# Kernel tuning notes

Hardware: AMD Instinct MI355X
Metric: run time of the kernel (lower is better)

The kernel has to match this reference:

```python
import jax, jax.numpy as jnp
import numpy as np

# Fixed-point emulation: SharedFxpShift = 8 -> scale 256. Integer bit-shifts of the
# original int32/int8 pipeline are emulated in float32 (multiply/divide by 2^8) with
# int8 clamping, keeping the same dataflow (resblock -> pred head -> bin packing ->
# upsample -> (N,8,ch) child scatter) so a quantized kernel can be checked against it.
SHIFT = 256.0

def requant(x):
    # RequantFxpToScaledInt8: shift down and clamp to int8 range
    return jnp.clip(x * (1.0 / SHIFT), -128.0, 127.0)

def prelu(x, a):
    return jnp.where(x >= 0, x, a * x)

def resblock(x, w1, w2, a):
    # SparseResBlockIn32W8Out32: requant -> linear -> prelu -> requant -> linear -> +x
    h = requant(x)
    h = h @ w1.T
    h = prelu(h, a)
    h = requant(h)
    h = h @ w2.T
    return x + h

def setup_inputs() -> dict:
    key = jax.random.key(0)
    ks = jax.random.split(key, 16)
    N, CH = 50000, 256
    w = lambda k, shp: jax.random.normal(k, shp, dtype=jnp.float32) * 0.05
    return {
        'x': jax.random.normal(ks[0], (N, CH), dtype=jnp.float32) * SHIFT,
        'cur_bin': jax.random.randint(ks[1], (N, 8), 0, 2, dtype=jnp.int32),
        'w_dec1': w(ks[2], (CH, CH)),
        'w_dec2': w(ks[3], (CH, CH)),
        'a_dec': jax.random.uniform(ks[4], (1,), dtype=jnp.float32),
        'w_pconv': w(ks[5], (CH, CH)),
        'a_pconv': jax.random.uniform(ks[6], (1,), dtype=jnp.float32),
        'w_plin': w(ks[7], (255, CH)),
        'w_up1': w(ks[8], (CH, CH + 8)),
        'a_up1': jax.random.uniform(ks[9], (1,), dtype=jnp.float32),
        'w_ur1': w(ks[10], (CH, CH)),
        'w_ur2': w(ks[11], (CH, CH)),
        'a_ur': jax.random.uniform(ks[12], (1,), dtype=jnp.float32),
        'w_uout': w(ks[13], (2048, CH)),
    }

def reference(x, cur_bin, w_dec1, w_dec2, a_dec, w_pconv, a_pconv, w_plin,
              w_up1, a_up1, w_ur1, w_ur2, a_ur, w_uout):
    N, CH = x.shape
    binf = cur_bin.astype(jnp.float32)
    # dec: residual block
    rec = resblock(x, w_dec1, w_dec2, a_dec)
    # pred: requant -> conv+prelu -> requant -> linear(ch,255)
    h = requant(rec)
    h = prelu(h @ w_pconv.T, a_pconv)
    h = requant(h)
    cur_pred = h @ w_plin.T                                   # [N, 255]
    # bin -> octree symbol: (cur_bin << arange(8)).sum(1) - 1
    bin2oct = jnp.arange(8, dtype=jnp.int32)
    cur_oct = jnp.sum(cur_bin << bin2oct, axis=1).astype(jnp.int16) - 1  # [N]
    # upsample: cat(rec, bin << shift) -> requant -> lin+prelu -> resblock -> requant -> lin(ch*8)
    u = jnp.concatenate([rec, binf * SHIFT], axis=1)          # [N, CH+8]
    u = requant(u)
    u = prelu(u @ w_up1.T, a_up1)
    u = resblock(u, w_ur1, w_ur2, a_ur)
    u = requant(u)
    u = u @ w_uout.T                                          # [N, 8*CH]
    # child gather: original does reshape(N,8,CH)[cur_bin.bool()] (ragged);
    # we keep the dense [N,8,CH] with unoccupied children zeroed (jit-friendly).
    rec_out = u.reshape(N, 8, CH) * binf[:, :, None]
    return rec_out, cur_pred, cur_oct
```

## Files before the change

kernel.cpp:

```cpp
#include <hip/hip_runtime.h>

typedef __bf16 bf16x8 __attribute__((ext_vector_type(8)));
typedef float  f32x4  __attribute__((ext_vector_type(4)));

#define OFF_DEC1  0
#define OFF_DEC2  65536
#define OFF_PCONV 131072
#define OFF_PLIN  196608
#define OFF_UP1   262144
#define OFF_UR1   335872
#define OFF_UR2   401408
#define OFF_UOUT  466944
#define WB_TOTAL  991232

__device__ __align__(16) unsigned short g_wb[WB_TOTAL];

__device__ __forceinline__ unsigned short f2bf(float f) {
  union { float f; unsigned u; } c; c.f = f;
  unsigned u = c.u + 0x7FFFu + ((c.u >> 16) & 1u);
  return (unsigned short)(u >> 16);
}
__device__ __forceinline__ float bf2f(unsigned short b) {
  union { unsigned u; float f; } c; c.u = ((unsigned)b) << 16;
  return c.f;
}
__device__ __forceinline__ float reqf(float v) {
  return fminf(fmaxf(v * 0.00390625f, -128.f), 127.f);
}

__global__ void wconv_kernel(const float* __restrict__ wd1, const float* __restrict__ wd2,
                             const float* __restrict__ wpc, const float* __restrict__ wpl,
                             const float* __restrict__ wu1, const float* __restrict__ wr1,
                             const float* __restrict__ wr2, const float* __restrict__ wuo) {
  int t = blockIdx.x * 256 + threadIdx.x;
  if (t >= WB_TOTAL) return;
  const float* src; int local, Ksrc = 256, Msrc = 256, rowOff = 0;
  if      (t < OFF_DEC2)  { src = wd1; local = t; }
  else if (t < OFF_PCONV) { src = wd2; local = t - OFF_DEC2; }
  else if (t < OFF_PLIN)  { src = wpc; local = t - OFF_PCONV; }
  else if (t < OFF_UP1)   { src = wpl; local = t - OFF_PLIN; Msrc = 255; }
  else if (t < OFF_UR1)   { src = wu1; local = t - OFF_UP1; Ksrc = 264; }
  else if (t < OFF_UR2)   { src = wr1; local = t - OFF_UR1; }
  else if (t < OFF_UOUT)  { src = wr2; local = t - OFF_UR2; }
  else { local = t - OFF_UOUT; int c = local >> 16; local &= 65535; src = wuo; rowOff = c * 256; }
  const int s = local >> 13, j = local & 8191;
  const int h = j >> 12, wv = (j >> 9) & 7, lq = (j >> 7) & 3;
  const int l15 = (j >> 3) & 15, kk = j & 7;
  const int m = wv * 32 + h * 16 + l15;
  const int k = s * 32 + lq * 8 + kk;
  float v = (m < Msrc && k < Ksrc) ? src[(size_t)(rowOff + m) * Ksrc + k] : 0.f;
  g_wb[t] = f2bf(v);
}


__device__ __forceinline__ void zero_acc(f32x4 (&acc)[2][4]) {
#pragma unroll
  for (int i = 0; i < 2; ++i)
#pragma unroll
    for (int j = 0; j < 4; ++j) acc[i][j] = (f32x4){0.f, 0.f, 0.f, 0.f};
}

__device__ __forceinline__ void prelu_acc(f32x4 (&acc)[2][4], float a) {
#pragma unroll
  for (int i = 0; i < 2; ++i)
#pragma unroll
    for (int j = 0; j < 4; ++j)
#pragma unroll
      for (int r = 0; r < 4; ++r) {
        float v = acc[i][j][r];
        acc[i][j][r] = v >= 0.f ? v : a * v;
      }
}

__device__ __forceinline__ void stageWh(const unsigned short* __restrict__ src,
                                        unsigned short* dst, int w, int l) {
  const int off = w * 512 + l * 8;
  __builtin_amdgcn_global_load_lds(
      (const __attribute__((address_space(1))) unsigned*)(src + off),
      (__attribute__((address_space(3))) unsigned*)(dst + off),
      16, 0, 0);
}

template<int NKS, bool BIN_TAIL>
__device__ __forceinline__ void gemm_ring(const unsigned short* __restrict__ wcur,
                                          const unsigned short* __restrict__ wnext,
                                          unsigned short* sW,
                                          const unsigned short* sAct,
                                          const unsigned short* sBinA,
                                          int w, int l, int l15, int lq,
                                          f32x4 (&acc)[2][4]) {
  bf16x8 af[4];
#pragma unroll
  for (int hs = 0; hs < 2 * NKS; ++hs) {
    const int ks = hs >> 1, mt = hs & 1;
    const int slot = hs & 1, nslot = slot ^ 1;
    if (hs + 1 < 2 * NKS) {
      stageWh(wcur + (hs + 1) * 4096, sW + nslot * 4096, w, l);
      asm volatile("s_waitcnt vmcnt(1)" ::: "memory");
    } else if (wnext) {
      stageWh(wnext, sW + nslot * 4096, w, l);
      asm volatile("s_waitcnt vmcnt(1)" ::: "memory");
    } else {
      asm volatile("s_waitcnt vmcnt(0)" ::: "memory");
    }
    __builtin_amdgcn_sched_barrier(0);
    if (mt == 0) {
      if (BIN_TAIL && ks == NKS - 1) {
#pragma unroll
        for (int nt = 0; nt < 4; ++nt)
          af[nt] = *(const bf16x8*)(sBinA + (nt * 16 + l15) * 32 + lq * 8);
      } else {
        const int kb = ks * 64 + lq * 16;
#pragma unroll
        for (int nt = 0; nt < 4; ++nt) {
          const int row = nt * 16 + l15;
          af[nt] = *(const bf16x8*)((const char*)sAct + row * 512 + (kb ^ ((row & 15) << 4)));
        }
      }
    }
    __builtin_amdgcn_s_setprio(1);
    bf16x8 bfr = *(const bf16x8*)(sW + slot * 4096 + w * 512 + lq * 128 + l15 * 8);
#pragma unroll
    for (int nt = 0; nt < 4; ++nt)
      acc[mt][nt] = __builtin_amdgcn_mfma_f32_16x16x32_bf16(bfr, af[nt], acc[mt][nt], 0, 0, 0);
    __builtin_amdgcn_s_setprio(0);
  }
}

__device__ __forceinline__ void stage_rq(const f32x4 (&acc)[2][4], unsigned short* dst,
                                         int w, int l15, int lq) {
#pragma unroll
  for (int nt = 0; nt < 4; ++nt) {
    const int row = nt * 16 + l15;
    const int swz = (row & 15) << 4;
#pragma unroll
    for (int mt = 0; mt < 2; ++mt) {
      const int ch2 = (w * 32 + mt * 16 + lq * 4) * 2;
      ushort4 b4;
      b4.x = f2bf(reqf(acc[mt][nt][0]));
      b4.y = f2bf(reqf(acc[mt][nt][1]));
      b4.z = f2bf(reqf(acc[mt][nt][2]));
      b4.w = f2bf(reqf(acc[mt][nt][3]));
      *(ushort4*)((char*)dst + row * 512 + (ch2 ^ swz)) = b4;
    }
  }
}

__device__ __forceinline__ void store_chunk(const f32x4 (&acc)[2][4], float* __restrict__ out,
                                            const unsigned short* sBinA, int r0, int N,
                                            int c, int w, int l15, int lq) {
#pragma unroll
  for (int nt = 0; nt < 4; ++nt) {
    const int row = nt * 16 + l15;
    if ((r0 + row) < N) {
      const float m = sBinA[row * 32 + c] ? 1.f : 0.f;
      float* rp = out + (size_t)(r0 + row) * 2048 + c * 256;
#pragma unroll
      for (int mt = 0; mt < 2; ++mt) {
        const int ch0 = w * 32 + mt * 16 + lq * 4;
        f32x4 v;
        v[0] = acc[mt][nt][0] * m; v[1] = acc[mt][nt][1] * m;
        v[2] = acc[mt][nt][2] * m; v[3] = acc[mt][nt][3] * m;
        *(f32x4*)(rp + ch0) = v;
      }
    }
  }
}

__global__ __launch_bounds__(512, 4) void fused_kernel(
    const float* __restrict__ x, const int* __restrict__ cur_bin,
    const float* __restrict__ a_dec, const float* __restrict__ a_pconv,
    const float* __restrict__ a_up1, const float* __restrict__ a_ur,
    float* __restrict__ out, int N)
{
  __shared__ __align__(16) unsigned short sA[64 * 256];
  __shared__ __align__(16) unsigned short sW[2 * 4096];
  __shared__ __align__(16) unsigned short sBinA[64 * 32];

  const int tid = threadIdx.x;
  const int w = tid >> 6, l = tid & 63;
  const int l15 = l & 15, lq = l >> 4;
  const int r0 = blockIdx.x * 64;
  const size_t PRED_BASE = (size_t)N * 2048;
  const size_t OCT_BASE  = PRED_BASE + (size_t)N * 255;

  const float A_DEC = a_dec[0], A_PCONV = a_pconv[0], A_UP1 = a_up1[0], A_UR = a_ur[0];

  stageWh(g_wb + OFF_DEC1, sW, w, l);

  for (int i = tid; i < 64 * 32; i += 512) {
    const int row = i >> 5, j = i & 31;
    float bv = 0.f;
    if (j < 8 && (r0 + row) < N) bv = (float)cur_bin[(size_t)(r0 + row) * 8 + j];
    sBinA[i] = (j < 8) ? f2bf(bv) : (unsigned short)0;
  }
  if (tid < 64 && (r0 + tid) < N) {
    int s = 0;
#pragma unroll
    for (int j = 0; j < 8; ++j) s += cur_bin[(size_t)(r0 + tid) * 8 + j] << j;
    out[OCT_BASE + r0 + tid] = (float)(s - 1);
  }
#pragma unroll
  for (int it = 0; it < 8; ++it) {
    const int e = it * 2048 + tid * 4;
    const int row = e >> 8, col = e & 255;
    float4 xv = make_float4(0.f, 0.f, 0.f, 0.f);
    if ((r0 + row) < N) xv = *(const float4*)(x + (size_t)(r0 + row) * 256 + col);
    ushort4 b4;
    b4.x = f2bf(reqf(xv.x)); b4.y = f2bf(reqf(xv.y));
    b4.z = f2bf(reqf(xv.z)); b4.w = f2bf(reqf(xv.w));
    *(ushort4*)((char*)sA + row * 512 + ((col * 2) ^ ((row & 15) << 4))) = b4;
  }
  __syncthreads();

  f32x4 acc[2][4];

  zero_acc(acc);
  gemm_ring<8, false>(g_wb + OFF_DEC1, g_wb + OFF_DEC2, sW, sA, sBinA, w, l, l15, lq, acc);
  prelu_acc(acc, A_DEC);
  __syncthreads();
  stage_rq(acc, sA, w, l15, lq);
  __syncthreads();

  zero_acc(acc);
  gemm_ring<8, false>(g_wb + OFF_DEC2, g_wb + OFF_UP1, sW, sA, sBinA, w, l, l15, lq, acc);
  __syncthreads();
#pragma unroll
  for (int nt = 0; nt < 4; ++nt) {
    const int row = nt * 16 + l15;
    const int swz = (row & 15) << 4;
#pragma unroll
    for (int mt = 0; mt < 2; ++mt) {
      const int ch0 = w * 32 + mt * 16 + lq * 4;
      float4 xv = make_float4(0.f, 0.f, 0.f, 0.f);
      if ((r0 + row) < N) xv = *(const float4*)(x + (size_t)(r0 + row) * 256 + ch0);
      ushort4 b4;
      b4.x = f2bf(reqf(xv.x + acc[mt][nt][0]));
      b4.y = f2bf(reqf(xv.y + acc[mt][nt][1]));
      b4.z = f2bf(reqf(xv.z + acc[mt][nt][2]));
      b4.w = f2bf(reqf(xv.w + acc[mt][nt][3]));
      *(ushort4*)((char*)sA + row * 512 + ((ch0 * 2) ^ swz)) = b4;
    }
  }
  __syncthreads();

  unsigned u1p[2][4][2];
  zero_acc(acc);
  gemm_ring<9, true>(g_wb + OFF_UP1, g_wb + OFF_PCONV, sW, sA, sBinA, w, l, l15, lq, acc);
  prelu_acc(acc, A_UP1);
#pragma unroll
  for (int i = 0; i < 2; ++i)
#pragma unroll
    for (int j = 0; j < 4; ++j)
#pragma unroll
      for (int p = 0; p < 2; ++p)
        u1p[i][j][p] = (unsigned)f2bf(acc[i][j][2 * p]) |
                       ((unsigned)f2bf(acc[i][j][2 * p + 1]) << 16);

  zero_acc(acc);
  gemm_ring<8, false>(g_wb + OFF_PCONV, g_wb + OFF_PLIN, sW, sA, sBinA, w, l, l15, lq, acc);
  prelu_acc(acc, A_PCONV);
  __syncthreads();
  stage_rq(acc, sA, w, l15, lq);
  __syncthreads();

  zero_acc(acc);
  gemm_ring<8, false>(g_wb + OFF_PLIN, g_wb + OFF_UR1, sW, sA, sBinA, w, l, l15, lq, acc);
#pragma unroll
  for (int nt = 0; nt < 4; ++nt) {
    const int row = nt * 16 + l15;
    if ((r0 + row) < N) {
      float* rp = out + PRED_BASE + (size_t)(r0 + row) * 255;
#pragma unroll
      for (int mt = 0; mt < 2; ++mt) {
        const int col0 = w * 32 + mt * 16 + lq * 4;
#pragma unroll
        for (int r = 0; r < 4; ++r)
          if (col0 + r < 255)
            rp[col0 + r] = acc[mt][nt][r];
      }
    }
  }
  __syncthreads();

#pragma unroll
  for (int nt = 0; nt < 4; ++nt) {
    const int row = nt * 16 + l15;
    const int swz = (row & 15) << 4;
#pragma unroll
    for (int mt = 0; mt < 2; ++mt) {
      const int ch2 = (w * 32 + mt * 16 + lq * 4) * 2;
      ushort4 b4;
      b4.x = f2bf(reqf(bf2f((unsigned short)(u1p[mt][nt][0]))));
      b4.y = f2bf(reqf(bf2f((unsigned short)(u1p[mt][nt][0] >> 16))));
      b4.z = f2bf(reqf(bf2f((unsigned short)(u1p[mt][nt][1]))));
      b4.w = f2bf(reqf(bf2f((unsigned short)(u1p[mt][nt][1] >> 16))));
      *(ushort4*)((char*)sA + row * 512 + (ch2 ^ swz)) = b4;
    }
  }
  __syncthreads();

  zero_acc(acc);
  gemm_ring<8, false>(g_wb + OFF_UR1, g_wb + OFF_UR2, sW, sA, sBinA, w, l, l15, lq, acc);
  prelu_acc(acc, A_UR);
  __syncthreads();
  stage_rq(acc, sA, w, l15, lq);
  __syncthreads();

  zero_acc(acc);
  gemm_ring<8, false>(g_wb + OFF_UR2, g_wb + OFF_UOUT, sW, sA, sBinA, w, l, l15, lq, acc);
#pragma unroll
  for (int i = 0; i < 2; ++i)
#pragma unroll
    for (int j = 0; j < 4; ++j) {
      acc[i][j][0] += bf2f((unsigned short)(u1p[i][j][0]));
      acc[i][j][1] += bf2f((unsigned short)(u1p[i][j][0] >> 16));
      acc[i][j][2] += bf2f((unsigned short)(u1p[i][j][1]));
      acc[i][j][3] += bf2f((unsigned short)(u1p[i][j][1] >> 16));
    }
  __syncthreads();
  stage_rq(acc, sA, w, l15, lq);
  __syncthreads();

#define G8_CHUNK(c, nextptr)                                                            \
  zero_acc(acc);                                                                        \
  gemm_ring<8, false>(g_wb + OFF_UOUT + (c) * 65536, nextptr, sW, sA, sBinA,            \
                      w, l, l15, lq, acc);                                              \
  store_chunk(acc, out, sBinA, r0, N, (c), w, l15, lq);

  G8_CHUNK(0, g_wb + OFF_UOUT + 1 * 65536)
  G8_CHUNK(1, g_wb + OFF_UOUT + 2 * 65536)
  G8_CHUNK(2, g_wb + OFF_UOUT + 3 * 65536)
  G8_CHUNK(3, g_wb + OFF_UOUT + 4 * 65536)
  G8_CHUNK(4, g_wb + OFF_UOUT + 5 * 65536)
  G8_CHUNK(5, g_wb + OFF_UOUT + 6 * 65536)
  G8_CHUNK(6, g_wb + OFF_UOUT + 7 * 65536)
  G8_CHUNK(7, (const unsigned short*)nullptr)
#undef G8_CHUNK
}

extern "C" void kernel_launch(void* const* d_in, const int* in_sizes, int n_in,
                              void* d_out, int out_size, void* d_ws, size_t ws_size,
                              hipStream_t stream) {
  const float* x        = (const float*)d_in[0];
  const int*   cur_bin  = (const int*)d_in[1];
  const float* w_dec1   = (const float*)d_in[2];
  const float* w_dec2   = (const float*)d_in[3];
  const float* a_dec    = (const float*)d_in[4];
  const float* w_pconv  = (const float*)d_in[5];
  const float* a_pconv  = (const float*)d_in[6];
  const float* w_plin   = (const float*)d_in[7];
  const float* w_up1    = (const float*)d_in[8];
  const float* a_up1    = (const float*)d_in[9];
  const float* w_ur1    = (const float*)d_in[10];
  const float* w_ur2    = (const float*)d_in[11];
  const float* a_ur     = (const float*)d_in[12];
  const float* w_uout   = (const float*)d_in[13];

  const int N = in_sizes[0] / 256;

  wconv_kernel<<<(WB_TOTAL + 255) / 256, 256, 0, stream>>>(
      w_dec1, w_dec2, w_pconv, w_plin, w_up1, w_ur1, w_ur2, w_uout);

  fused_kernel<<<(N + 63) / 64, 512, 0, stream>>>(
      x, cur_bin, a_dec, a_pconv, a_up1, a_ur, (float*)d_out, N);
}
```

Measured before the change: 277.4 us.

## Prefetch weights through registers two k-steps ahead instead of async LDS ring

Replaces the per-half-step global_load_lds double buffer with a register-staged pipeline. Each wave loads its weight slice for k-step ks+2 into registers and writes the slice for ks+1 into a private LDS slot. The packed weight layout is reordered so one k-step holds both M sub-tiles per wave, and the weight LDS buffer doubles in size. The aim is to remove the vmcnt waits and sched barriers on every half-step and to overlap global latency with more MFMA work. The cost is extra VGPRs and more LDS per block, which can lower occupancy or cause spills.

```diff
diff --git a/kernel.cpp b/kernel.cpp
--- a/kernel.cpp
+++ b/kernel.cpp
@@ -44,9 +44,9 @@
   else if (t < OFF_UOUT)  { src = wr2; local = t - OFF_UR2; }
   else { local = t - OFF_UOUT; int c = local >> 16; local &= 65535; src = wuo; rowOff = c * 256; }
   const int s = local >> 13, j = local & 8191;
-  const int h = j >> 12, wv = (j >> 9) & 7, lq = (j >> 7) & 3;
+  const int wv = j >> 10, lq = (j >> 8) & 3, mt = (j >> 7) & 1;
   const int l15 = (j >> 3) & 15, kk = j & 7;
-  const int m = wv * 32 + h * 16 + l15;
+  const int m = wv * 32 + mt * 16 + l15;
   const int k = s * 32 + lq * 8 + kk;
   float v = (m < Msrc && k < Ksrc) ? src[(size_t)(rowOff + m) * Ksrc + k] : 0.f;
   g_wb[t] = f2bf(v);
@@ -72,58 +72,51 @@
       }
 }
 
-__device__ __forceinline__ void stageWh(const unsigned short* __restrict__ src,
-                                        unsigned short* dst, int w, int l) {
-  const int off = w * 512 + l * 8;
-  __builtin_amdgcn_global_load_lds(
-      (const __attribute__((address_space(1))) unsigned*)(src + off),
-      (__attribute__((address_space(3))) unsigned*)(dst + off),
-      16, 0, 0);
-}
-
-template<int NKS, bool BIN_TAIL>
-__device__ __forceinline__ void gemm_ring(const unsigned short* __restrict__ wcur,
-                                          const unsigned short* __restrict__ wnext,
-                                          unsigned short* sW,
-                                          const unsigned short* sAct,
-                                          const unsigned short* sBinA,
-                                          int w, int l, int l15, int lq,
-                                          f32x4 (&acc)[2][4]) {
-  bf16x8 af[4];
-#pragma unroll
-  for (int hs = 0; hs < 2 * NKS; ++hs) {
-    const int ks = hs >> 1, mt = hs & 1;
-    const int slot = hs & 1, nslot = slot ^ 1;
-    if (hs + 1 < 2 * NKS) {
-      stageWh(wcur + (hs + 1) * 4096, sW + nslot * 4096, w, l);
-      asm volatile("s_waitcnt vmcnt(1)" ::: "memory");
-    } else if (wnext) {
-      stageWh(wnext, sW + nslot * 4096, w, l);
-      asm volatile("s_waitcnt vmcnt(1)" ::: "memory");
+template<int NKS, bool BIN_TAIL, int PH>
+__device__ __forceinline__ void gemm_rs(const unsigned short* __restrict__ wcur,
+                                        const unsigned short* __restrict__ wnext,
+                                        bf16x8 (&wr)[2][2],
+                                        unsigned short* sW,
+                                        const unsigned short* sAct,
+                                        const unsigned short* sBinA,
+                                        int w, int l, int l15, int lq,
+                                        f32x4 (&acc)[2][4]) {
+  const int off = w * 1024 + l * 8;
+#pragma unroll
+  for (int ks = 0; ks < NKS; ++ks) {
+    const int cur = (PH + ks) & 1;
+    const int nxt = cur ^ 1;
+    if (ks + 1 < NKS || wnext != nullptr) {
+      *(bf16x8*)(sW + nxt * 8192 + off)       = wr[nxt][0];
+      *(bf16x8*)(sW + nxt * 8192 + off + 512) = wr[nxt][1];
+    }
+    const unsigned short* nsrc = nullptr;
+    if (ks + 2 < NKS)      nsrc = wcur + (ks + 2) * 8192;
+    else if (wnext)        nsrc = wnext + (ks + 2 - NKS) * 8192;
+    if (nsrc) {
+      wr[cur][0] = *(const bf16x8*)(nsrc + off);
+      wr[cur][1] = *(const bf16x8*)(nsrc + off + 512);
+    }
+    bf16x8 af[4];
+    if (BIN_TAIL && ks == NKS - 1) {
+#pragma unroll
+      for (int nt = 0; nt < 4; ++nt)
+        af[nt] = *(const bf16x8*)(sBinA + (nt * 16 + l15) * 32 + lq * 8);
     } else {
-      asm volatile("s_waitcnt vmcnt(0)" ::: "memory");
-    }
-    __builtin_amdgcn_sched_barrier(0);
-    if (mt == 0) {
-      if (BIN_TAIL && ks == NKS - 1) {
-#pragma unroll
-        for (int nt = 0; nt < 4; ++nt)
-          af[nt] = *(const bf16x8*)(sBinA + (nt * 16 + l15) * 32 + lq * 8);
-      } else {
-        const int kb = ks * 64 + lq * 16;
-#pragma unroll
-        for (int nt = 0; nt < 4; ++nt) {
-          const int row = nt * 16 + l15;
-          af[nt] = *(const bf16x8*)((const char*)sAct + row * 512 + (kb ^ ((row & 15) << 4)));
-        }
+      const int kb = ks * 64 + lq * 16;
+#pragma unroll
+      for (int nt = 0; nt < 4; ++nt) {
+        const int row = nt * 16 + l15;
+        af[nt] = *(const bf16x8*)((const char*)sAct + row * 512 + (kb ^ ((row & 15) << 4)));
       }
     }
-    __builtin_amdgcn_s_setprio(1);
-    bf16x8 bfr = *(const bf16x8*)(sW + slot * 4096 + w * 512 + lq * 128 + l15 * 8);
-#pragma unroll
-    for (int nt = 0; nt < 4; ++nt)
-      acc[mt][nt] = __builtin_amdgcn_mfma_f32_16x16x32_bf16(bfr, af[nt], acc[mt][nt], 0, 0, 0);
-    __builtin_amdgcn_s_setprio(0);
+#pragma unroll
+    for (int mt = 0; mt < 2; ++mt) {
+      bf16x8 bfr = *(const bf16x8*)(sW + cur * 8192 + w * 1024 + lq * 256 + mt * 128 + l15 * 8);
+#pragma unroll
+      for (int nt = 0; nt < 4; ++nt)
+        acc[mt][nt] = __builtin_amdgcn_mfma_f32_16x16x32_bf16(bfr, af[nt], acc[mt][nt], 0, 0, 0);
+    }
   }
 }
 
@@ -146,27 +139,6 @@
   }
 }
 
-__device__ __forceinline__ void store_chunk(const f32x4 (&acc)[2][4], float* __restrict__ out,
-                                            const unsigned short* sBinA, int r0, int N,
-                                            int c, int w, int l15, int lq) {
-#pragma unroll
-  for (int nt = 0; nt < 4; ++nt) {
-    const int row = nt * 16 + l15;
-    if ((r0 + row) < N) {
-      const float m = sBinA[row * 32 + c] ? 1.f : 0.f;
-      float* rp = out + (size_t)(r0 + row) * 2048 + c * 256;
-#pragma unroll
-      for (int mt = 0; mt < 2; ++mt) {
-        const int ch0 = w * 32 + mt * 16 + lq * 4;
-        f32x4 v;
-        v[0] = acc[mt][nt][0] * m; v[1] = acc[mt][nt][1] * m;
-        v[2] = acc[mt][nt][2] * m; v[3] = acc[mt][nt][3] * m;
-        *(f32x4*)(rp + ch0) = v;
-      }
-    }
-  }
-}
-
 __global__ __launch_bounds__(512, 4) void fused_kernel(
     const float* __restrict__ x, const int* __restrict__ cur_bin,
     const float* __restrict__ a_dec, const float* __restrict__ a_pconv,
@@ -174,7 +146,7 @@
     float* __restrict__ out, int N)
 {
   __shared__ __align__(16) unsigned short sA[64 * 256];
-  __shared__ __align__(16) unsigned short sW[2 * 4096];
+  __shared__ __align__(16) unsigned short sW[2 * 8192];
   __shared__ __align__(16) unsigned short sBinA[64 * 32];
 
   const int tid = threadIdx.x;
@@ -186,7 +158,12 @@
 
   const float A_DEC = a_dec[0], A_PCONV = a_pconv[0], A_UP1 = a_up1[0], A_UR = a_ur[0];
 
-  stageWh(g_wb + OFF_DEC1, sW, w, l);
+  const int woff = w * 1024 + l * 8;
+  bf16x8 wr[2][2];
+  wr[0][0] = *(const bf16x8*)(g_wb + OFF_DEC1 + woff);
+  wr[0][1] = *(const bf16x8*)(g_wb + OFF_DEC1 + woff + 512);
+  wr[1][0] = *(const bf16x8*)(g_wb + OFF_DEC1 + 8192 + woff);
+  wr[1][1] = *(const bf16x8*)(g_wb + OFF_DEC1 + 8192 + woff + 512);
 
   for (int i = tid; i < 64 * 32; i += 512) {
     const int row = i >> 5, j = i & 31;
@@ -200,7 +177,7 @@
     for (int j = 0; j < 8; ++j) s += cur_bin[(size_t)(r0 + tid) * 8 + j] << j;
     out[OCT_BASE + r0 + tid] = (float)(s - 1);
   }
-#pragma unroll
+#pragma unroll 1
   for (int it = 0; it < 8; ++it) {
     const int e = it * 2048 + tid * 4;
     const int row = e >> 8, col = e & 255;
@@ -213,17 +190,20 @@
   }
   __syncthreads();
 
+  *(bf16x8*)(sW + woff)       = wr[0][0];
+  *(bf16x8*)(sW + woff + 512) = wr[0][1];
+
   f32x4 acc[2][4];
 
   zero_acc(acc);
-  gemm_ring<8, false>(g_wb + OFF_DEC1, g_wb + OFF_DEC2, sW, sA, sBinA, w, l, l15, lq, acc);
+  gemm_rs<8, false, 0>(g_wb + OFF_DEC1, g_wb + OFF_DEC2, wr, sW, sA, sBinA, w, l, l15, lq, acc);
   prelu_acc(acc, A_DEC);
   __syncthreads();
   stage_rq(acc, sA, w, l15, lq);
   __syncthreads();
 
   zero_acc(acc);
-  gemm_ring<8, false>(g_wb + OFF_DEC2, g_wb + OFF_UP1, sW, sA, sBinA, w, l, l15, lq, acc);
+  gemm_rs<8, false, 0>(g_wb + OFF_DEC2, g_wb + OFF_UP1, wr, sW, sA, sBinA, w, l, l15, lq, acc);
   __syncthreads();
 #pragma unroll
   for (int nt = 0; nt < 4; ++nt) {
@@ -246,7 +226,7 @@
 
   unsigned u1p[2][4][2];
   zero_acc(acc);
-  gemm_ring<9, true>(g_wb + OFF_UP1, g_wb + OFF_PCONV, sW, sA, sBinA, w, l, l15, lq, acc);
+  gemm_rs<9, true, 0>(g_wb + OFF_UP1, g_wb + OFF_PCONV, wr, sW, sA, sBinA, w, l, l15, lq, acc);
   prelu_acc(acc, A_UP1);
 #pragma unroll
   for (int i = 0; i < 2; ++i)
@@ -258,14 +238,14 @@
                        ((unsigned)f2bf(acc[i][j][2 * p + 1]) << 16);
 
   zero_acc(acc);
-  gemm_ring<8, false>(g_wb + OFF_PCONV, g_wb + OFF_PLIN, sW, sA, sBinA, w, l, l15, lq, acc);
+  gemm_rs<8, false, 1>(g_wb + OFF_PCONV, g_wb + OFF_PLIN, wr, sW, sA, sBinA, w, l, l15, lq, acc);
   prelu_acc(acc, A_PCONV);
   __syncthreads();
   stage_rq(acc, sA, w, l15, lq);
   __syncthreads();
 
   zero_acc(acc);
-  gemm_ring<8, false>(g_wb + OFF_PLIN, g_wb + OFF_UR1, sW, sA, sBinA, w, l, l15, lq, acc);
+  gemm_rs<8, false, 1>(g_wb + OFF_PLIN, g_wb + OFF_UR1, wr, sW, sA, sBinA, w, l, l15, lq, acc);
 #pragma unroll
   for (int nt = 0; nt < 4; ++nt) {
     const int row = nt * 16 + l15;
@@ -301,14 +281,14 @@
   __syncthreads();
 
   zero_acc(acc);
-  gemm_ring<8, false>(g_wb + OFF_UR1, g_wb + OFF_UR2, sW, sA, sBinA, w, l, l15, lq, acc);
+  gemm_rs<8, false, 1>(g_wb + OFF_UR1, g_wb + OFF_UR2, wr, sW, sA, sBinA, w, l, l15, lq, acc);
   prelu_acc(acc, A_UR);
   __syncthreads();
   stage_rq(acc, sA, w, l15, lq);
   __syncthreads();
 
   zero_acc(acc);
-  gemm_ring<8, false>(g_wb + OFF_UR2, g_wb + OFF_UOUT, sW, sA, sBinA, w, l, l15, lq, acc);
+  gemm_rs<8, false, 1>(g_wb + OFF_UR2, g_wb + OFF_UOUT, wr, sW, sA, sBinA, w, l, l15, lq, acc);
 #pragma unroll
   for (int i = 0; i < 2; ++i)
 #pragma unroll
@@ -324,9 +304,26 @@
 
 #define G8_CHUNK(c, nextptr)                                                            \
   zero_acc(acc);                                                                        \
-  gemm_ring<8, false>(g_wb + OFF_UOUT + (c) * 65536, nextptr, sW, sA, sBinA,            \
-                      w, l, l15, lq, acc);                                              \
-  store_chunk(acc, out, sBinA, r0, N, (c), w, l15, lq);
+  gemm_rs<8, false, 1>(g_wb + OFF_UOUT + (c) * 65536, nextptr, wr, sW, sA, sBinA,       \
+                       w, l, l15, lq, acc);                                             \
+  {                                                                                     \
+    _Pragma("unroll")                                                                   \
+    for (int nt = 0; nt < 4; ++nt) {                                                    \
+      const int row = nt * 16 + l15;                                                    \
+      if ((r0 + row) < N) {                                                             \
+        const float m = sBinA[row * 32 + (c)] ? 1.f : 0.f;                              \
+        float* rp = out + (size_t)(r0 + row) * 2048 + (c) * 256;                        \
+        _Pragma("unroll")                                                               \
+        for (int mt = 0; mt < 2; ++mt) {                                                \
+          const int ch0 = w * 32 + mt * 16 + lq * 4;                                    \
+          f32x4 v;                                                                      \
+          v[0] = acc[mt][nt][0] * m; v[1] = acc[mt][nt][1] * m;                         \
+          v[2] = acc[mt][nt][2] * m; v[3] = acc[mt][nt][3] * m;                         \
+          *(f32x4*)(rp + ch0) = v;                                                      \
+        }                                                                               \
+      }                                                                                 \
+    }                                                                                   \
+  }
 
   G8_CHUNK(0, g_wb + OFF_UOUT + 1 * 65536)
   G8_CHUNK(1, g_wb + OFF_UOUT + 2 * 65536)
```

New measurement: 324.7 us. +17.0%, slower.
